# Kernel optimization log

Hardware: AMD Instinct MI355X
Metric: run time of the kernel (lower is better)

## Reference

```python
import jax, jax.numpy as jnp
import numpy as np

N_NODES = 50000
N_EDGES = 800000
NFEAT = 96
NHID = 128
EPS = 1e-12  # F.normalize default eps


def setup_inputs() -> dict:
    key = jax.random.key(0)
    k1, k2, k3, k4 = jax.random.split(key, 4)
    edge_index = jax.random.randint(k1, (2, N_EDGES), 0, N_NODES, dtype=jnp.int64)
    x = jax.random.normal(k2, (N_NODES, NFEAT), dtype=jnp.float32)
    # Glorot-ish scaling for linear weights
    W_l = jax.random.normal(k3, (NHID, NFEAT), dtype=jnp.float32) * (1.0 / np.sqrt(NFEAT))
    b_l = jnp.zeros((NHID,), dtype=jnp.float32)
    W_r = jax.random.normal(k4, (NHID, NFEAT), dtype=jnp.float32) * (1.0 / np.sqrt(NFEAT))
    return {"edge_index": edge_index, "x": x, "W_l": W_l, "b_l": b_l, "W_r": W_r}


def reference(edge_index, x, W_l, b_l, W_r):
    # PyG SAGEConv, aggr='mean', root_weight=True, normalize=True
    src, dst = edge_index[0], edge_index[1]
    # gather source features, scatter-sum into destination nodes
    msg_sum = jax.ops.segment_sum(x[src], dst, num_segments=N_NODES)  # [N, nfeat]
    deg = jax.ops.segment_sum(jnp.ones((edge_index.shape[1],), dtype=x.dtype),
                              dst, num_segments=N_NODES)
    agg = msg_sum / jnp.maximum(deg, 1.0)[:, None]  # mean; isolated nodes -> 0
    out = agg @ W_l.T + b_l + x @ W_r.T  # [N, nhid]
    # L2 normalize per node (F.normalize p=2, dim=-1)
    norm = jnp.linalg.norm(out, axis=-1, keepdims=True)
    return out / jnp.maximum(norm, EPS)
```

## Files before the change

kernel.cpp:

```cpp
#include <hip/hip_runtime.h>


typedef __attribute__((ext_vector_type(8))) short short8;
typedef __attribute__((ext_vector_type(4))) float floatx4;

constexpr int kNodes = 50000;
constexpr int kEdges = 800000;
constexpr int kF = 96;
constexpr int kH = 128;
constexpr int kEllW = 32;
constexpr int kSpillCap = 4096;
constexpr int kBktRange = kNodes / 8;

constexpr size_t kXhOff    = 0;
constexpr size_t kAggOff   = 9600000;
constexpr size_t kWhOff    = 19200000;
constexpr size_t kEllOff   = 19249152;
constexpr size_t kCurOff   = 22449152;
constexpr size_t kSpcOff   = 22649152;
constexpr size_t kSpillOff = 22649168;

__device__ __forceinline__ unsigned pack2_bf16(float a, float b) {
  unsigned ua = __float_as_uint(a), ub = __float_as_uint(b);
  ua = (ua + 0x7fffu + ((ua >> 16) & 1u)) >> 16;
  ub = (ub + 0x7fffu + ((ub >> 16) & 1u)) >> 16;
  return ua | (ub << 16);
}
__device__ __forceinline__ float bf_lo(unsigned u) { return __uint_as_float(u << 16); }
__device__ __forceinline__ float bf_hi(unsigned u) { return __uint_as_float(u & 0xffff0000u); }

__device__ __forceinline__ void ell_insert(int dst, int src, int* cursor,
                                           ushort* ell, unsigned* spill,
                                           int* spillCnt) {
  const int slot = atomicAdd(&cursor[dst], 1);
  if (slot < kEllW) {
    ell[(size_t)dst * kEllW + slot] = (ushort)src;
  } else {
    const int sp = atomicAdd(spillCnt, 1);
    if (sp < kSpillCap) spill[sp] = ((unsigned)dst << 16) | (unsigned)src;
  }
}

__global__ void __launch_bounds__(256)
prep_kernel(const float* __restrict__ x, const float* __restrict__ Wl,
            const float* __restrict__ Wr, uint4* __restrict__ xh4,
            uint4* __restrict__ wh4, uint4* __restrict__ zero4) {
  constexpr int kCvt = kNodes * kF / 8;
  constexpr int kWcvt = kH * 192 / 8;
  constexpr int kZero = 12501;
  const int i = blockIdx.x * 256 + threadIdx.x;
  if (i < kCvt) {
    const float4 v0 = reinterpret_cast<const float4*>(x)[i * 2];
    const float4 v1 = reinterpret_cast<const float4*>(x)[i * 2 + 1];
    uint4 o;
    o.x = pack2_bf16(v0.x, v0.y);
    o.y = pack2_bf16(v0.z, v0.w);
    o.z = pack2_bf16(v1.x, v1.y);
    o.w = pack2_bf16(v1.z, v1.w);
    xh4[i] = o;
  } else if (i < kCvt + kWcvt) {
    const int j = i - kCvt;
    const int row = j / 24, chunk = j % 24;
    const float* src = (chunk < 12) ? (Wl + (size_t)row * kF + chunk * 8)
                                    : (Wr + (size_t)row * kF + (chunk - 12) * 8);
    const float4 v0 = reinterpret_cast<const float4*>(src)[0];
    const float4 v1 = reinterpret_cast<const float4*>(src)[1];
    uint4 o;
    o.x = pack2_bf16(v0.x, v0.y);
    o.y = pack2_bf16(v0.z, v0.w);
    o.z = pack2_bf16(v1.x, v1.y);
    o.w = pack2_bf16(v1.z, v1.w);
    wh4[j] = o;
  } else if (i < kCvt + kWcvt + kZero) {
    zero4[i - kCvt - kWcvt] = make_uint4(0, 0, 0, 0);
  }
}

__global__ void __launch_bounds__(256)
fill_kernel(const int* __restrict__ ei, int* __restrict__ cursor,
            ushort* __restrict__ ell, unsigned* __restrict__ spill,
            int* __restrict__ spillCnt) {
  const int g = blockIdx.x & 7;
  const int chunk = blockIdx.x >> 3;
  const int lo = g * kBktRange, hi = lo + kBktRange;
  const int base = chunk * 1024 + threadIdx.x;
  int d[4];
#pragma unroll
  for (int k = 0; k < 4; ++k) {
    const int e = base + k * 256;
    d[k] = (e < kEdges) ? ei[kEdges + e] : -1;
  }
#pragma unroll
  for (int k = 0; k < 4; ++k) {
    if (d[k] >= lo && d[k] < hi) {
      const int e = base + k * 256;
      ell_insert(d[k], ei[e], cursor, ell, spill, spillCnt);
    }
  }
}

__global__ void __launch_bounds__(256)
gather_kernel(const uint4* __restrict__ xh4, const int* __restrict__ cursor,
              const ushort* __restrict__ ell, const unsigned* __restrict__ spill,
              const int* __restrict__ spillCnt, uint4* __restrict__ aggh4) {
  const int wave = threadIdx.x >> 6, lane = threadIdx.x & 63;
  const int slot = lane / 12;
  const int c = lane % 12;
  const bool gactive = lane < 48;
  const int sc = min(*spillCnt, kSpillCap);
  const int g = blockIdx.x & 7;
  const int j = blockIdx.x >> 3;
  const int stride = (gridDim.x >> 3) * 4;
  const int hi = (g + 1) * kBktRange;

  for (int node = g * kBktRange + j * 4 + wave; node < hi; node += stride) {
    const int deg = cursor[node];
    const int dmain = min(deg, kEllW);
    const ushort* __restrict__ erow = ell + (size_t)node * kEllW;
    float a0 = 0.f, a1 = 0.f, a2 = 0.f, a3 = 0.f,
          a4 = 0.f, a5 = 0.f, a6 = 0.f, a7 = 0.f;

    int srcs[8];
#pragma unroll
    for (int t = 0; t < 8; ++t) {
      const int idx = (t << 2) + slot;
      srcs[t] = (gactive && idx < dmain) ? (int)erow[idx] : -1;
    }
#pragma unroll
    for (int t = 0; t < 8; ++t) {
      if (srcs[t] >= 0) {
        const uint4 v = xh4[(size_t)srcs[t] * 12 + c];
        a0 += bf_lo(v.x); a1 += bf_hi(v.x);
        a2 += bf_lo(v.y); a3 += bf_hi(v.y);
        a4 += bf_lo(v.z); a5 += bf_hi(v.z);
        a6 += bf_lo(v.w); a7 += bf_hi(v.w);
      }
    }
    for (int jj = 0; jj < sc; ++jj) {
      const unsigned pr = spill[jj];
      if ((int)(pr >> 16) == node && lane < 12) {
        const uint4 v = xh4[(size_t)(pr & 0xffffu) * 12 + c];
        a0 += bf_lo(v.x); a1 += bf_hi(v.x);
        a2 += bf_lo(v.y); a3 += bf_hi(v.y);
        a4 += bf_lo(v.z); a5 += bf_hi(v.z);
        a6 += bf_lo(v.w); a7 += bf_hi(v.w);
      }
    }
    a0 += __shfl(a0, lane + 24, 64); a1 += __shfl(a1, lane + 24, 64);
    a2 += __shfl(a2, lane + 24, 64); a3 += __shfl(a3, lane + 24, 64);
    a4 += __shfl(a4, lane + 24, 64); a5 += __shfl(a5, lane + 24, 64);
    a6 += __shfl(a6, lane + 24, 64); a7 += __shfl(a7, lane + 24, 64);
    a0 += __shfl(a0, lane + 12, 64); a1 += __shfl(a1, lane + 12, 64);
    a2 += __shfl(a2, lane + 12, 64); a3 += __shfl(a3, lane + 12, 64);
    a4 += __shfl(a4, lane + 12, 64); a5 += __shfl(a5, lane + 12, 64);
    a6 += __shfl(a6, lane + 12, 64); a7 += __shfl(a7, lane + 12, 64);

    if (lane < 12) {
      const float inv = 1.0f / fmaxf((float)deg, 1.0f);
      uint4 o;
      o.x = pack2_bf16(a0 * inv, a1 * inv);
      o.y = pack2_bf16(a2 * inv, a3 * inv);
      o.z = pack2_bf16(a4 * inv, a5 * inv);
      o.w = pack2_bf16(a6 * inv, a7 * inv);
      aggh4[(size_t)node * 12 + c] = o;
    }
  }
}

__global__ void __launch_bounds__(256)
mfma_kernel(const uint4* __restrict__ xh4, const uint4* __restrict__ aggh4,
            const uint4* __restrict__ wh4, const float* __restrict__ bl,
            float* __restrict__ out) {
  const int wave = threadIdx.x >> 6, lane = threadIdx.x & 63;
  const int tile = blockIdx.x * 4 + wave;
  if (tile >= kNodes / 16) return;
  const int base = tile * 16;
  const int r = lane & 15, q = lane >> 4;

  const short8* aggS = reinterpret_cast<const short8*>(aggh4);
  const short8* xhS  = reinterpret_cast<const short8*>(xh4);
  const short8* whS  = reinterpret_cast<const short8*>(wh4);

  floatx4 acc[8] = {};
#pragma unroll
  for (int ks = 0; ks < 6; ++ks) {
    const short8* Ab = (ks < 3) ? aggS : xhS;
    const int chunk = (ks < 3 ? ks * 4 : (ks - 3) * 4) + q;
    const short8 a = Ab[(size_t)(base + r) * 12 + chunk];
#pragma unroll
    for (int cg = 0; cg < 8; ++cg) {
      const short8 b = whS[(cg * 16 + r) * 24 + ks * 4 + q];
      acc[cg] = __builtin_amdgcn_mfma_f32_16x16x32_bf16(a, b, acc[cg], 0, 0, 0);
    }
  }

  float p0 = 0.f, p1 = 0.f, p2 = 0.f, p3 = 0.f;
#pragma unroll
  for (int cg = 0; cg < 8; ++cg) {
    const float bb = bl[cg * 16 + r];
    acc[cg][0] += bb; acc[cg][1] += bb; acc[cg][2] += bb; acc[cg][3] += bb;
    p0 += acc[cg][0] * acc[cg][0];
    p1 += acc[cg][1] * acc[cg][1];
    p2 += acc[cg][2] * acc[cg][2];
    p3 += acc[cg][3] * acc[cg][3];
  }
#pragma unroll
  for (int off = 1; off < 16; off <<= 1) {
    p0 += __shfl_xor(p0, off, 64);
    p1 += __shfl_xor(p1, off, 64);
    p2 += __shfl_xor(p2, off, 64);
    p3 += __shfl_xor(p3, off, 64);
  }
  const float s0 = 1.0f / fmaxf(sqrtf(p0), 1e-12f);
  const float s1 = 1.0f / fmaxf(sqrtf(p1), 1e-12f);
  const float s2 = 1.0f / fmaxf(sqrtf(p2), 1e-12f);
  const float s3 = 1.0f / fmaxf(sqrtf(p3), 1e-12f);

#pragma unroll
  for (int cg = 0; cg < 8; ++cg) {
    const int col = cg * 16 + r;
    float* o = out + (size_t)(base + q * 4) * kH + col;
    o[0 * kH] = acc[cg][0] * s0;
    o[1 * kH] = acc[cg][1] * s1;
    o[2 * kH] = acc[cg][2] * s2;
    o[3 * kH] = acc[cg][3] * s3;
  }
}

extern "C" void kernel_launch(void* const* d_in, const int* in_sizes, int n_in,
                              void* d_out, int out_size, void* d_ws, size_t ws_size,
                              hipStream_t stream) {
  const int*   ei = (const int*)d_in[0];
  const float* x  = (const float*)d_in[1];
  const float* Wl = (const float*)d_in[2];
  const float* bl = (const float*)d_in[3];
  const float* Wr = (const float*)d_in[4];
  float* out = (float*)d_out;

  char* ws = (char*)d_ws;
  uint4*    xh4      = (uint4*)(ws + kXhOff);
  uint4*    aggh4    = (uint4*)(ws + kAggOff);
  uint4*    wh4      = (uint4*)(ws + kWhOff);
  ushort*   ell      = (ushort*)(ws + kEllOff);
  int*      cursor   = (int*)(ws + kCurOff);
  int*      spillCnt = (int*)(ws + kSpcOff);
  unsigned* spill    = (unsigned*)(ws + kSpillOff);

  constexpr int kPrepTotal = kNodes * kF / 8 + kH * 192 / 8 + 12501;
  prep_kernel<<<(kPrepTotal + 255) / 256, 256, 0, stream>>>(
      x, Wl, Wr, xh4, wh4, (uint4*)(ws + kCurOff));

  fill_kernel<<<782 * 8, 256, 0, stream>>>(ei, cursor, ell, spill, spillCnt);

  gather_kernel<<<391 * 8, 256, 0, stream>>>(xh4, cursor, ell, spill, spillCnt,
                                             aggh4);

  constexpr int tiles = kNodes / 16;
  mfma_kernel<<<(tiles + 3) / 4, 256, 0, stream>>>(xh4, aggh4, wh4, bl, out);
}
```

Measured before the change: 112.7 us.

## Fuse ELL fill with bf16 conversion and process two nodes per wave in gather

Merges the edge-bucketing fill kernel and the x/W bf16 conversion into one launch, with block ranges choosing the role, and moves cursor/spill zeroing to a hipMemsetAsync. The fill blocks can then overlap with the conversion traffic, and one serialized kernel boundary disappears. The gather kernel now handles two destination nodes per wave iteration so more independent row gathers are in flight. This doubles the accumulator registers, which may lower occupancy, and adds a memset call to the launch sequence.

```diff
diff --git a/kernel.cpp b/kernel.cpp
--- a/kernel.cpp
+++ b/kernel.cpp
@@ -19,6 +19,10 @@
 constexpr size_t kCurOff   = 22449152;
 constexpr size_t kSpcOff   = 22649152;
 constexpr size_t kSpillOff = 22649168;
+
+constexpr int kFillBlocks = 782 * 8;
+constexpr int kPrepItems  = kNodes * kF / 8 + kH * 192 / 8;
+constexpr int kPrepBlocks = (kPrepItems + 255) / 256;
 
 __device__ __forceinline__ unsigned pack2_bf16(float a, float b) {
   unsigned ua = __float_as_uint(a), ub = __float_as_uint(b);
@@ -42,13 +46,33 @@
 }
 
 __global__ void __launch_bounds__(256)
-prep_kernel(const float* __restrict__ x, const float* __restrict__ Wl,
-            const float* __restrict__ Wr, uint4* __restrict__ xh4,
-            uint4* __restrict__ wh4, uint4* __restrict__ zero4) {
+mega_kernel(const int* __restrict__ ei, const float* __restrict__ x,
+            const float* __restrict__ Wl, const float* __restrict__ Wr,
+            uint4* __restrict__ xh4, uint4* __restrict__ wh4,
+            int* __restrict__ cursor, ushort* __restrict__ ell,
+            unsigned* __restrict__ spill, int* __restrict__ spillCnt) {
+  if (blockIdx.x < kFillBlocks) {
+    const int g = blockIdx.x & 7;
+    const int chunk = blockIdx.x >> 3;
+    const int lo = g * kBktRange, hi = lo + kBktRange;
+    const int base = chunk * 1024 + threadIdx.x;
+    int d[4];
+#pragma unroll
+    for (int k = 0; k < 4; ++k) {
+      const int e = base + k * 256;
+      d[k] = (e < kEdges) ? ei[kEdges + e] : -1;
+    }
+#pragma unroll
+    for (int k = 0; k < 4; ++k) {
+      if (d[k] >= lo && d[k] < hi) {
+        const int e = base + k * 256;
+        ell_insert(d[k], ei[e], cursor, ell, spill, spillCnt);
+      }
+    }
+    return;
+  }
   constexpr int kCvt = kNodes * kF / 8;
-  constexpr int kWcvt = kH * 192 / 8;
-  constexpr int kZero = 12501;
-  const int i = blockIdx.x * 256 + threadIdx.x;
+  const int i = (blockIdx.x - kFillBlocks) * 256 + threadIdx.x;
   if (i < kCvt) {
     const float4 v0 = reinterpret_cast<const float4*>(x)[i * 2];
     const float4 v1 = reinterpret_cast<const float4*>(x)[i * 2 + 1];
@@ -58,7 +82,7 @@
     o.z = pack2_bf16(v1.x, v1.y);
     o.w = pack2_bf16(v1.z, v1.w);
     xh4[i] = o;
-  } else if (i < kCvt + kWcvt) {
+  } else if (i < kPrepItems) {
     const int j = i - kCvt;
     const int row = j / 24, chunk = j % 24;
     const float* src = (chunk < 12) ? (Wl + (size_t)row * kF + chunk * 8)
@@ -71,31 +95,6 @@
     o.z = pack2_bf16(v1.x, v1.y);
     o.w = pack2_bf16(v1.z, v1.w);
     wh4[j] = o;
-  } else if (i < kCvt + kWcvt + kZero) {
-    zero4[i - kCvt - kWcvt] = make_uint4(0, 0, 0, 0);
-  }
-}
-
-__global__ void __launch_bounds__(256)
-fill_kernel(const int* __restrict__ ei, int* __restrict__ cursor,
-            ushort* __restrict__ ell, unsigned* __restrict__ spill,
-            int* __restrict__ spillCnt) {
-  const int g = blockIdx.x & 7;
-  const int chunk = blockIdx.x >> 3;
-  const int lo = g * kBktRange, hi = lo + kBktRange;
-  const int base = chunk * 1024 + threadIdx.x;
-  int d[4];
-#pragma unroll
-  for (int k = 0; k < 4; ++k) {
-    const int e = base + k * 256;
-    d[k] = (e < kEdges) ? ei[kEdges + e] : -1;
-  }
-#pragma unroll
-  for (int k = 0; k < 4; ++k) {
-    if (d[k] >= lo && d[k] < hi) {
-      const int e = base + k * 256;
-      ell_insert(d[k], ei[e], cursor, ell, spill, spillCnt);
-    }
   }
 }
 
@@ -110,40 +109,64 @@
   const int sc = min(*spillCnt, kSpillCap);
   const int g = blockIdx.x & 7;
   const int j = blockIdx.x >> 3;
-  const int stride = (gridDim.x >> 3) * 4;
+  const int stride = (gridDim.x >> 3) * 8;
   const int hi = (g + 1) * kBktRange;
 
-  for (int node = g * kBktRange + j * 4 + wave; node < hi; node += stride) {
-    const int deg = cursor[node];
-    const int dmain = min(deg, kEllW);
-    const ushort* __restrict__ erow = ell + (size_t)node * kEllW;
+  for (int nA = g * kBktRange + j * 8 + wave * 2; nA < hi; nA += stride) {
+    const int nB = nA + 1;
+    const bool hasB = nB < hi;
+    const int degA = cursor[nA];
+    const int degB = hasB ? cursor[nB] : 0;
+    const int dmA = min(degA, kEllW);
+    const int dmB = min(degB, kEllW);
+    const ushort* __restrict__ erowA = ell + (size_t)nA * kEllW;
+    const ushort* __restrict__ erowB = ell + (size_t)nB * kEllW;
+
     float a0 = 0.f, a1 = 0.f, a2 = 0.f, a3 = 0.f,
           a4 = 0.f, a5 = 0.f, a6 = 0.f, a7 = 0.f;
-
-    int srcs[8];
+    float b0 = 0.f, b1 = 0.f, b2 = 0.f, b3 = 0.f,
+          b4 = 0.f, b5 = 0.f, b6 = 0.f, b7 = 0.f;
+
+    int sA[8], sB[8];
 #pragma unroll
     for (int t = 0; t < 8; ++t) {
       const int idx = (t << 2) + slot;
-      srcs[t] = (gactive && idx < dmain) ? (int)erow[idx] : -1;
+      sA[t] = (gactive && idx < dmA) ? (int)erowA[idx] : -1;
+      sB[t] = (gactive && idx < dmB) ? (int)erowB[idx] : -1;
     }
 #pragma unroll
     for (int t = 0; t < 8; ++t) {
-      if (srcs[t] >= 0) {
-        const uint4 v = xh4[(size_t)srcs[t] * 12 + c];
+      if (sA[t] >= 0) {
+        const uint4 v = xh4[(size_t)sA[t] * 12 + c];
         a0 += bf_lo(v.x); a1 += bf_hi(v.x);
         a2 += bf_lo(v.y); a3 += bf_hi(v.y);
         a4 += bf_lo(v.z); a5 += bf_hi(v.z);
         a6 += bf_lo(v.w); a7 += bf_hi(v.w);
       }
+      if (sB[t] >= 0) {
+        const uint4 v = xh4[(size_t)sB[t] * 12 + c];
+        b0 += bf_lo(v.x); b1 += bf_hi(v.x);
+        b2 += bf_lo(v.y); b3 += bf_hi(v.y);
+        b4 += bf_lo(v.z); b5 += bf_hi(v.z);
+        b6 += bf_lo(v.w); b7 += bf_hi(v.w);
+      }
     }
     for (int jj = 0; jj < sc; ++jj) {
       const unsigned pr = spill[jj];
-      if ((int)(pr >> 16) == node && lane < 12) {
+      const int pd = (int)(pr >> 16);
+      if (lane < 12 && (pd == nA || (hasB && pd == nB))) {
         const uint4 v = xh4[(size_t)(pr & 0xffffu) * 12 + c];
-        a0 += bf_lo(v.x); a1 += bf_hi(v.x);
-        a2 += bf_lo(v.y); a3 += bf_hi(v.y);
-        a4 += bf_lo(v.z); a5 += bf_hi(v.z);
-        a6 += bf_lo(v.w); a7 += bf_hi(v.w);
+        if (pd == nA) {
+          a0 += bf_lo(v.x); a1 += bf_hi(v.x);
+          a2 += bf_lo(v.y); a3 += bf_hi(v.y);
+          a4 += bf_lo(v.z); a5 += bf_hi(v.z);
+          a6 += bf_lo(v.w); a7 += bf_hi(v.w);
+        } else {
+          b0 += bf_lo(v.x); b1 += bf_hi(v.x);
+          b2 += bf_lo(v.y); b3 += bf_hi(v.y);
+          b4 += bf_lo(v.z); b5 += bf_hi(v.z);
+          b6 += bf_lo(v.w); b7 += bf_hi(v.w);
+        }
       }
     }
     a0 += __shfl(a0, lane + 24, 64); a1 += __shfl(a1, lane + 24, 64);
@@ -154,15 +177,32 @@
     a2 += __shfl(a2, lane + 12, 64); a3 += __shfl(a3, lane + 12, 64);
     a4 += __shfl(a4, lane + 12, 64); a5 += __shfl(a5, lane + 12, 64);
     a6 += __shfl(a6, lane + 12, 64); a7 += __shfl(a7, lane + 12, 64);
+    b0 += __shfl(b0, lane + 24, 64); b1 += __shfl(b1, lane + 24, 64);
+    b2 += __shfl(b2, lane + 24, 64); b3 += __shfl(b3, lane + 24, 64);
+    b4 += __shfl(b4, lane + 24, 64); b5 += __shfl(b5, lane + 24, 64);
+    b6 += __shfl(b6, lane + 24, 64); b7 += __shfl(b7, lane + 24, 64);
+    b0 += __shfl(b0, lane + 12, 64); b1 += __shfl(b1, lane + 12, 64);
+    b2 += __shfl(b2, lane + 12, 64); b3 += __shfl(b3, lane + 12, 64);
+    b4 += __shfl(b4, lane + 12, 64); b5 += __shfl(b5, lane + 12, 64);
+    b6 += __shfl(b6, lane + 12, 64); b7 += __shfl(b7, lane + 12, 64);
 
     if (lane < 12) {
-      const float inv = 1.0f / fmaxf((float)deg, 1.0f);
+      const float invA = 1.0f / fmaxf((float)degA, 1.0f);
       uint4 o;
-      o.x = pack2_bf16(a0 * inv, a1 * inv);
-      o.y = pack2_bf16(a2 * inv, a3 * inv);
-      o.z = pack2_bf16(a4 * inv, a5 * inv);
-      o.w = pack2_bf16(a6 * inv, a7 * inv);
-      aggh4[(size_t)node * 12 + c] = o;
+      o.x = pack2_bf16(a0 * invA, a1 * invA);
+      o.y = pack2_bf16(a2 * invA, a3 * invA);
+      o.z = pack2_bf16(a4 * invA, a5 * invA);
+      o.w = pack2_bf16(a6 * invA, a7 * invA);
+      aggh4[(size_t)nA * 12 + c] = o;
+      if (hasB) {
+        const float invB = 1.0f / fmaxf((float)degB, 1.0f);
+        uint4 p;
+        p.x = pack2_bf16(b0 * invB, b1 * invB);
+        p.y = pack2_bf16(b2 * invB, b3 * invB);
+        p.z = pack2_bf16(b4 * invB, b5 * invB);
+        p.w = pack2_bf16(b6 * invB, b7 * invB);
+        aggh4[(size_t)nB * 12 + c] = p;
+      }
     }
   }
 }
@@ -246,11 +286,10 @@
   int*      spillCnt = (int*)(ws + kSpcOff);
   unsigned* spill    = (unsigned*)(ws + kSpillOff);
 
-  constexpr int kPrepTotal = kNodes * kF / 8 + kH * 192 / 8 + 12501;
-  prep_kernel<<<(kPrepTotal + 255) / 256, 256, 0, stream>>>(
-      x, Wl, Wr, xh4, wh4, (uint4*)(ws + kCurOff));
-
-  fill_kernel<<<782 * 8, 256, 0, stream>>>(ei, cursor, ell, spill, spillCnt);
+  hipMemsetAsync(ws + kCurOff, 0, 200008, stream);
+
+  mega_kernel<<<kFillBlocks + kPrepBlocks, 256, 0, stream>>>(
+      ei, x, Wl, Wr, xh4, wh4, cursor, ell, spill, spillCnt);
 
   gather_kernel<<<391 * 8, 256, 0, stream>>>(xh4, cursor, ell, spill, spillCnt,
                                              aggh4);
```

New measurement: 111.7 us. About the same (-0.9%).
